# Kernel optimization log

Measured on AMD Instinct MI355X. Metric: run time of the kernel, lower is better.

The kernel has to match this reference:

```python
import jax, jax.numpy as jnp
import numpy as np
from jax import lax

D = 96        # voxel grid side
C = 16        # code_dim == inner channels
NCONV = 17    # total conv layers in the net
DN = ('NCDHW', 'OIDHW', 'NCDHW')
PAD1 = [(1, 1)] * 3


def _bn_relu_mask(y, s, b, mask):
    # eval-mode BN folded to scale/bias, ReLU, then restrict to active voxels
    s = s[None, :, None, None, None]
    b = b[None, :, None, None, None]
    return jnp.maximum(y * s + b, 0.0) * mask


def _subm(x, mask, w, s, b):
    # SubMConv3d: dense 3x3x3 conv on zero-padded sparse features, output only at
    # the (unchanged) active sites -> conv + mask is exactly equal math.
    y = lax.conv_general_dilated(x, w, (1, 1, 1), PAD1, dimension_numbers=DN)
    return _bn_relu_mask(y, s, b, mask)


def _down(x, mask, w, s, b):
    # SparseConv3d stride 2, pad 1: output active wherever any input in the 3^3
    # window is active (= max-pool of the mask).
    y = lax.conv_general_dilated(x, w, (2, 2, 2), PAD1, dimension_numbers=DN)
    new_mask = lax.reduce_window(mask, 0.0, lax.max, (1, 1, 3, 3, 3),
                                 (1, 1, 2, 2, 2),
                                 [(0, 0), (0, 0), (1, 1), (1, 1), (1, 1)])
    return _bn_relu_mask(y, s, b, new_mask), new_mask


def setup_inputs() -> dict:
    key = jax.random.key(0)
    k1, k2, k3, k4, k5 = jax.random.split(key, 5)
    mask_idx = jax.random.randint(k1, (1, 1, D, D, D), 0, 10, dtype=jnp.int32)
    mask = (mask_idx == 0).astype(jnp.float32)
    x = jax.random.normal(k2, (1, C, D, D, D), jnp.float32) * mask
    # 0.05 ~ 1/sqrt(27*16): keeps activations sane over 17 layers
    W = jax.random.normal(k3, (NCONV, C, C, 3, 3, 3), jnp.float32) * 0.05
    bn_scale = jax.random.uniform(k4, (NCONV, C), jnp.float32, 0.5, 1.5)
    bn_bias = jax.random.normal(k5, (NCONV, C), jnp.float32) * 0.1
    return {"x": x, "mask_idx": mask_idx, "W": W,
            "bn_scale": bn_scale, "bn_bias": bn_bias}


def reference(x, mask_idx, W, bn_scale, bn_bias):
    mask = (mask_idx == 0).astype(x.dtype)
    net = x
    i = 0
    # conv0: double_conv at full res
    for _ in range(2):
        net = _subm(net, mask, W[i], bn_scale[i], bn_bias[i]); i += 1
    # down0
    net, mask = _down(net, mask, W[i], bn_scale[i], bn_bias[i]); i += 1
    # conv1: double_conv -> net1.dense()
    for _ in range(2):
        net = _subm(net, mask, W[i], bn_scale[i], bn_bias[i]); i += 1
    net1 = net
    # down1 + conv2 (triple) -> net2
    net, mask = _down(net, mask, W[i], bn_scale[i], bn_bias[i]); i += 1
    for _ in range(3):
        net = _subm(net, mask, W[i], bn_scale[i], bn_bias[i]); i += 1
    net2 = net
    # down2 + conv3 (triple) -> net3
    net, mask = _down(net, mask, W[i], bn_scale[i], bn_bias[i]); i += 1
    for _ in range(3):
        net = _subm(net, mask, W[i], bn_scale[i], bn_bias[i]); i += 1
    net3 = net
    # down3 + conv4 (triple) -> net4
    net, mask = _down(net, mask, W[i], bn_scale[i], bn_bias[i]); i += 1
    for _ in range(3):
        net = _subm(net, mask, W[i], bn_scale[i], bn_bias[i]); i += 1
    net4 = net
    return (net1, net2, net3, net4)
```

## Files before the change

kernel.cpp:

```cpp
#include <hip/hip_runtime.h>

#define C 16
#define TAPS 27
#define NCONV 17
#define LISTCAP 98304
#define NPAIR 14

typedef _Float16 half8 __attribute__((ext_vector_type(8)));
typedef _Float16 half4 __attribute__((ext_vector_type(4)));
typedef float f32x4 __attribute__((ext_vector_type(4)));

__global__ void wh_kernel(const float* __restrict__ W, _Float16* __restrict__ Wh) {
    int i = blockIdx.x * blockDim.x + threadIdx.x;
    const int total = NCONV * NPAIR * 64 * 8;
    if (i >= total) return;
    int j = i & 7;
    int lane = (i >> 3) & 63;
    int p = (i >> 9) % NPAIR;
    int l = (i >> 9) / NPAIR;
    int co = lane & 15;
    int g = lane >> 4;
    int k = 8 * g + j;
    int ci = k & 15;
    int tap = 2 * p + (k >> 4);
    float val = (tap < TAPS) ? W[((l * C + co) * C + ci) * TAPS + tap] : 0.f;
    Wh[i] = (_Float16)val;
}

__global__ void transpose_in_h(const float* __restrict__ x, _Float16* __restrict__ xt, int n) {
    int v = blockIdx.x * blockDim.x + threadIdx.x;
    if (v >= n) return;
    half8 h0, h1;
#pragma unroll
    for (int c = 0; c < 8; c++) h0[c] = (_Float16)x[(long)c * n + v];
#pragma unroll
    for (int c = 0; c < 8; c++) h1[c] = (_Float16)x[(long)(c + 8) * n + v];
    half8* dp = reinterpret_cast<half8*>(xt + (long)v * C);
    dp[0] = h0;
    dp[1] = h1;
}

__global__ void to_ncdhw_h(const _Float16* __restrict__ src, float* __restrict__ dst, int n) {
    int v = blockIdx.x * blockDim.x + threadIdx.x;
    if (v >= n) return;
    const half8* sp = reinterpret_cast<const half8*>(src + (long)v * C);
    half8 q0 = sp[0], q1 = sp[1];
#pragma unroll
    for (int c = 0; c < 8; c++) dst[(long)c * n + v] = (float)q0[c];
#pragma unroll
    for (int c = 0; c < 8; c++) dst[(long)(c + 8) * n + v] = (float)q1[c];
}

__global__ void count_kernel(const int* __restrict__ mi, int* __restrict__ counts, int n) {
    int i = blockIdx.x * 256 + threadIdx.x;
    int act = (i < n) && (mi[i] == 0);
    unsigned long long b = __ballot(act);
    __shared__ int wsum[4];
    int wid = threadIdx.x >> 6, lane = threadIdx.x & 63;
    if (lane == 0) wsum[wid] = __popcll(b);
    __syncthreads();
    if (threadIdx.x == 0) counts[blockIdx.x] = wsum[0] + wsum[1] + wsum[2] + wsum[3];
}

__global__ void scan_kernel(const int* __restrict__ counts, int* __restrict__ offsets,
                            int* __restrict__ nact, int nb) {
    __shared__ int s[256];
    int t = threadIdx.x;
    const int CH = (nb + 255) / 256;
    int base = t * CH, sum = 0;
    for (int j = 0; j < CH; j++)
        if (base + j < nb) sum += counts[base + j];
    s[t] = sum;
    __syncthreads();
    for (int off = 1; off < 256; off <<= 1) {
        int v = (t >= off) ? s[t - off] : 0;
        __syncthreads();
        s[t] += v;
        __syncthreads();
    }
    int run = s[t] - sum;
    for (int j = 0; j < CH; j++) {
        if (base + j < nb) {
            offsets[base + j] = run;
            run += counts[base + j];
        }
    }
    if (t == 255) *nact = s[255];
}

__global__ void scatter_kernel(const int* __restrict__ mi, const int* __restrict__ offsets,
                               int* __restrict__ list, int n, int cap) {
    int i = blockIdx.x * 256 + threadIdx.x;
    int act = (i < n) && (mi[i] == 0);
    unsigned long long b = __ballot(act);
    __shared__ int wsum[4];
    int wid = threadIdx.x >> 6, lane = threadIdx.x & 63;
    if (lane == 0) wsum[wid] = __popcll(b);
    __syncthreads();
    int wbase = 0;
    for (int w = 0; w < wid; w++) wbase += wsum[w];
    int prefix = __popcll(b & ((1ull << lane) - 1));
    if (act) {
        int pos = offsets[blockIdx.x] + wbase + prefix;
        if (pos < cap) list[pos] = i;
    }
}

template <bool FROM_INT>
__global__ void pool_mask_kernel(const int* __restrict__ mi, const float* __restrict__ mf,
                                 float* __restrict__ mout, int Din, int Dout) {
    int i = blockIdx.x * blockDim.x + threadIdx.x;
    int n = Dout * Dout * Dout;
    if (i >= n) return;
    int x = i % Dout, y = (i / Dout) % Dout, z = i / (Dout * Dout);
    float v = 0.f;
    for (int kz = 0; kz < 3; kz++) {
        int zz = 2 * z - 1 + kz;
        if (zz < 0 || zz >= Din) continue;
        for (int ky = 0; ky < 3; ky++) {
            int yy = 2 * y - 1 + ky;
            if (yy < 0 || yy >= Din) continue;
            for (int kx = 0; kx < 3; kx++) {
                int xx = 2 * x - 1 + kx;
                if (xx < 0 || xx >= Din) continue;
                long idx = ((long)zz * Din + yy) * Din + xx;
                float mv = FROM_INT ? ((mi[idx] == 0) ? 1.f : 0.f) : mf[idx];
                v = fmaxf(v, mv);
            }
        }
    }
    mout[i] = v;
}

template <int STRIDE, bool SPARSE>
__global__ __launch_bounds__(256) void mconv_kernel(
    const _Float16* __restrict__ in, _Float16* __restrict__ out,
    const float* __restrict__ mask, const int* __restrict__ list,
    const int* __restrict__ nact, const _Float16* __restrict__ Whl,
    const float* __restrict__ bs, const float* __restrict__ bb,
    int Din, int Dout) {
    int n = Dout * Dout * Dout;
    int nv;
    if (SPARSE) {
        nv = *nact;
        if (nv > LISTCAP) nv = LISTCAP;
    } else {
        nv = n;
    }
    int tile = blockIdx.x * 4 + (threadIdx.x >> 6);
    if (tile * 16 >= nv) return;

    int lane = threadIdx.x & 63;
    int col = lane & 15;
    int g = lane >> 4;
    int s = tile * 16 + col;
    bool val = s < nv;
    int v = 0;
    if (SPARSE) {
        if (val) v = list[s];
    } else {
        v = val ? s : 0;
    }
    int x = v % Dout, y = (v / Dout) % Dout, z = v / (Dout * Dout);

    const half8* wf = reinterpret_cast<const half8*>(Whl);
    half8 a[NPAIR];
#pragma unroll
    for (int p = 0; p < NPAIR; p++) a[p] = wf[p * 64 + lane];

    int half_off = (g & 1) * 8;
    int tg = g >> 1;

    f32x4 acc = {0.f, 0.f, 0.f, 0.f};
#pragma unroll
    for (int p = 0; p < NPAIR; p++) {
        int tap = 2 * p + tg;
        if (tap > TAPS - 1) tap = TAPS - 1;
        int kz = tap / 9, ky = (tap / 3) % 3, kx = tap % 3;
        int zz = STRIDE * z - 1 + kz;
        int yy = STRIDE * y - 1 + ky;
        int xx = STRIDE * x - 1 + kx;
        bool ok = val && ((unsigned)zz < (unsigned)Din) && ((unsigned)yy < (unsigned)Din) &&
                  ((unsigned)xx < (unsigned)Din);
        half8 b = {};
        if (ok) {
            b = *reinterpret_cast<const half8*>(
                in + (long)((zz * Din + yy) * Din + xx) * C + half_off);
        }
        acc = __builtin_amdgcn_mfma_f32_16x16x32_f16(a[p], b, acc, 0, 0, 0);
    }

    if (val) {
        float mk = SPARSE ? 1.f : mask[v];
        int cob = g * 4;
        half4 r;
#pragma unroll
        for (int j = 0; j < 4; j++) {
            float t = fmaxf(acc[j] * bs[cob + j] + bb[cob + j], 0.f) * mk;
            r[j] = (_Float16)t;
        }
        *reinterpret_cast<half4*>(out + (long)v * C + cob) = r;
    }
}

extern "C" void kernel_launch(void* const* d_in, const int* in_sizes, int n_in,
                              void* d_out, int out_size, void* d_ws, size_t ws_size,
                              hipStream_t stream) {
    const float* x = (const float*)d_in[0];
    const int* mask_idx = (const int*)d_in[1];
    const float* W = (const float*)d_in[2];
    const float* bs = (const float*)d_in[3];
    const float* bb = (const float*)d_in[4];
    float* out = (float*)d_out;

    const int n96 = 96 * 96 * 96;
    const int n48 = 48 * 48 * 48;
    const int n24 = 24 * 24 * 24;
    const int n12 = 12 * 12 * 12;
    const int n6 = 6 * 6 * 6;
    const int NB = (n96 + 255) / 256;

    _Float16* P0h = (_Float16*)d_ws;
    _Float16* P1h = P0h + (long)C * n96;
    float* m48 = (float*)(P1h + (long)C * n96);
    float* m24 = m48 + n48;
    float* m12 = m24 + n24;
    float* m6 = m12 + n12;
    _Float16* Wh = (_Float16*)(m6 + n6);
    int* list = (int*)(Wh + (long)NCONV * NPAIR * 64 * 8);
    int* counts = list + LISTCAP;
    int* offsets = counts + NB;
    int* nact = offsets + NB;

    const int BS = 256;
    auto blk = [&](long t) { return dim3((unsigned)((t + BS - 1) / BS)); };
    auto mblk = [&](long nvox) { return dim3((unsigned)((nvox + 63) / 64)); };

    hipMemsetAsync(P1h, 0, (long)C * n96 * sizeof(_Float16), stream);
    hipLaunchKernelGGL(wh_kernel, blk(NCONV * NPAIR * 64 * 8), dim3(BS), 0, stream, W, Wh);
    hipLaunchKernelGGL(transpose_in_h, blk(n96), dim3(BS), 0, stream, x, P0h, n96);
    hipLaunchKernelGGL(count_kernel, dim3(NB), dim3(BS), 0, stream, mask_idx, counts, n96);
    hipLaunchKernelGGL(scan_kernel, dim3(1), dim3(BS), 0, stream, counts, offsets, nact, NB);
    hipLaunchKernelGGL(scatter_kernel, dim3(NB), dim3(BS), 0, stream, mask_idx, offsets, list,
                       n96, LISTCAP);

    auto sconv = [&](const _Float16* in, _Float16* op, int layer) {
        hipLaunchKernelGGL((mconv_kernel<1, true>), mblk(LISTCAP), dim3(BS), 0, stream,
                           in, op, (const float*)nullptr, list, nact,
                           Wh + (long)layer * NPAIR * 64 * 8, bs + layer * C, bb + layer * C,
                           96, 96);
    };
    auto subm = [&](const _Float16* in, _Float16* op, const float* m, int layer, int D) {
        int n = D * D * D;
        hipLaunchKernelGGL((mconv_kernel<1, false>), mblk(n), dim3(BS), 0, stream,
                           in, op, m, list, nact, Wh + (long)layer * NPAIR * 64 * 8,
                           bs + layer * C, bb + layer * C, D, D);
    };
    auto down = [&](const _Float16* in, _Float16* op, const float* m, int layer, int Dout) {
        int n = Dout * Dout * Dout;
        hipLaunchKernelGGL((mconv_kernel<2, false>), mblk(n), dim3(BS), 0, stream,
                           in, op, m, list, nact, Wh + (long)layer * NPAIR * 64 * 8,
                           bs + layer * C, bb + layer * C, 2 * Dout, Dout);
    };

    hipLaunchKernelGGL((pool_mask_kernel<true>), blk(n48), dim3(BS), 0, stream,
                       mask_idx, (const float*)nullptr, m48, 96, 48);
    hipLaunchKernelGGL((pool_mask_kernel<false>), blk(n24), dim3(BS), 0, stream,
                       (const int*)nullptr, m48, m24, 48, 24);
    hipLaunchKernelGGL((pool_mask_kernel<false>), blk(n12), dim3(BS), 0, stream,
                       (const int*)nullptr, m24, m12, 24, 12);
    hipLaunchKernelGGL((pool_mask_kernel<false>), blk(n6), dim3(BS), 0, stream,
                       (const int*)nullptr, m12, m6, 12, 6);

    sconv(P0h, P1h, 0);
    sconv(P1h, P0h, 1);
    down(P0h, P1h, m48, 2, 48);
    subm(P1h, P0h, m48, 3, 48);
    subm(P0h, P1h, m48, 4, 48);
    hipLaunchKernelGGL(to_ncdhw_h, blk(n48), dim3(BS), 0, stream, P1h, out, n48);
    down(P1h, P0h, m24, 5, 24);
    subm(P0h, P1h, m24, 6, 24);
    subm(P1h, P0h, m24, 7, 24);
    subm(P0h, P1h, m24, 8, 24);
    hipLaunchKernelGGL(to_ncdhw_h, blk(n24), dim3(BS), 0, stream, P1h, out + (long)C * n48, n24);
    down(P1h, P0h, m12, 9, 12);
    subm(P0h, P1h, m12, 10, 12);
    subm(P1h, P0h, m12, 11, 12);
    subm(P0h, P1h, m12, 12, 12);
    hipLaunchKernelGGL(to_ncdhw_h, blk(n12), dim3(BS), 0, stream, P1h,
                       out + (long)C * (n48 + n24), n12);
    down(P1h, P0h, m6, 13, 6);
    subm(P0h, P1h, m6, 14, 6);
    subm(P1h, P0h, m6, 15, 6);
    subm(P0h, P1h, m6, 16, 6);
    hipLaunchKernelGGL(to_ncdhw_h, blk(n6), dim3(BS), 0, stream, P1h,
                       out + (long)C * (n48 + n24 + n12), n6);
}
```

Measured before the change: 226.8 us.

## Fuse prep kernels, pooling, NCDHW writes, and low-res tail into single kernels

```diff
diff --git a/kernel.cpp b/kernel.cpp
--- a/kernel.cpp
+++ b/kernel.cpp
@@ -10,56 +10,50 @@
 typedef _Float16 half4 __attribute__((ext_vector_type(4)));
 typedef float f32x4 __attribute__((ext_vector_type(4)));
 
-__global__ void wh_kernel(const float* __restrict__ W, _Float16* __restrict__ Wh) {
-    int i = blockIdx.x * blockDim.x + threadIdx.x;
-    const int total = NCONV * NPAIR * 64 * 8;
-    if (i >= total) return;
-    int j = i & 7;
-    int lane = (i >> 3) & 63;
-    int p = (i >> 9) % NPAIR;
-    int l = (i >> 9) / NPAIR;
-    int co = lane & 15;
-    int g = lane >> 4;
-    int k = 8 * g + j;
-    int ci = k & 15;
-    int tap = 2 * p + (k >> 4);
-    float val = (tap < TAPS) ? W[((l * C + co) * C + ci) * TAPS + tap] : 0.f;
-    Wh[i] = (_Float16)val;
-}
-
-__global__ void transpose_in_h(const float* __restrict__ x, _Float16* __restrict__ xt, int n) {
-    int v = blockIdx.x * blockDim.x + threadIdx.x;
-    if (v >= n) return;
-    half8 h0, h1;
-#pragma unroll
-    for (int c = 0; c < 8; c++) h0[c] = (_Float16)x[(long)c * n + v];
-#pragma unroll
-    for (int c = 0; c < 8; c++) h1[c] = (_Float16)x[(long)(c + 8) * n + v];
-    half8* dp = reinterpret_cast<half8*>(xt + (long)v * C);
-    dp[0] = h0;
-    dp[1] = h1;
-}
-
-__global__ void to_ncdhw_h(const _Float16* __restrict__ src, float* __restrict__ dst, int n) {
-    int v = blockIdx.x * blockDim.x + threadIdx.x;
-    if (v >= n) return;
-    const half8* sp = reinterpret_cast<const half8*>(src + (long)v * C);
-    half8 q0 = sp[0], q1 = sp[1];
-#pragma unroll
-    for (int c = 0; c < 8; c++) dst[(long)c * n + v] = (float)q0[c];
-#pragma unroll
-    for (int c = 0; c < 8; c++) dst[(long)(c + 8) * n + v] = (float)q1[c];
-}
-
-__global__ void count_kernel(const int* __restrict__ mi, int* __restrict__ counts, int n) {
-    int i = blockIdx.x * 256 + threadIdx.x;
-    int act = (i < n) && (mi[i] == 0);
-    unsigned long long b = __ballot(act);
-    __shared__ int wsum[4];
-    int wid = threadIdx.x >> 6, lane = threadIdx.x & 63;
-    if (lane == 0) wsum[wid] = __popcll(b);
-    __syncthreads();
-    if (threadIdx.x == 0) counts[blockIdx.x] = wsum[0] + wsum[1] + wsum[2] + wsum[3];
+__global__ void prep_kernel(const float* __restrict__ x, const int* __restrict__ mask_idx,
+                            _Float16* __restrict__ P0h, _Float16* __restrict__ P1h,
+                            const float* __restrict__ W, _Float16* __restrict__ Wh,
+                            int* __restrict__ counts) {
+    const int n96 = 96 * 96 * 96;
+    int b = blockIdx.x;
+    if (b < 3456) {
+        int v = b * 256 + threadIdx.x;
+        half8 h0, h1;
+#pragma unroll
+        for (int c = 0; c < 8; c++) h0[c] = (_Float16)x[(long)c * n96 + v];
+#pragma unroll
+        for (int c = 0; c < 8; c++) h1[c] = (_Float16)x[(long)(c + 8) * n96 + v];
+        half8* dp = reinterpret_cast<half8*>(P0h + (long)v * C);
+        dp[0] = h0;
+        dp[1] = h1;
+        half8 zz = {};
+        half8* zp = reinterpret_cast<half8*>(P1h + (long)v * C);
+        zp[0] = zz;
+        zp[1] = zz;
+        int act = (mask_idx[v] == 0);
+        unsigned long long bl = __ballot(act);
+        __shared__ int wsum[4];
+        int wid = threadIdx.x >> 6, lane = threadIdx.x & 63;
+        if (lane == 0) wsum[wid] = __popcll(bl);
+        __syncthreads();
+        if (threadIdx.x == 0) counts[b] = wsum[0] + wsum[1] + wsum[2] + wsum[3];
+    } else {
+        int i = (b - 3456) * 256 + threadIdx.x;
+        const int total = NCONV * NPAIR * 64 * 8;
+        if (i < total) {
+            int j = i & 7;
+            int lane = (i >> 3) & 63;
+            int p = (i >> 9) % NPAIR;
+            int l = (i >> 9) / NPAIR;
+            int co = lane & 15;
+            int g = lane >> 4;
+            int k = 8 * g + j;
+            int ci = k & 15;
+            int tap = 2 * p + (k >> 4);
+            float val = (tap < TAPS) ? W[((l * C + co) * C + ci) * TAPS + tap] : 0.f;
+            Wh[i] = (_Float16)val;
+        }
+    }
 }
 
 __global__ void scan_kernel(const int* __restrict__ counts, int* __restrict__ offsets,
@@ -106,39 +100,65 @@
     }
 }
 
-template <bool FROM_INT>
-__global__ void pool_mask_kernel(const int* __restrict__ mi, const float* __restrict__ mf,
-                                 float* __restrict__ mout, int Din, int Dout) {
-    int i = blockIdx.x * blockDim.x + threadIdx.x;
-    int n = Dout * Dout * Dout;
-    if (i >= n) return;
-    int x = i % Dout, y = (i / Dout) % Dout, z = i / (Dout * Dout);
-    float v = 0.f;
-    for (int kz = 0; kz < 3; kz++) {
-        int zz = 2 * z - 1 + kz;
-        if (zz < 0 || zz >= Din) continue;
-        for (int ky = 0; ky < 3; ky++) {
-            int yy = 2 * y - 1 + ky;
-            if (yy < 0 || yy >= Din) continue;
-            for (int kx = 0; kx < 3; kx++) {
-                int xx = 2 * x - 1 + kx;
-                if (xx < 0 || xx >= Din) continue;
-                long idx = ((long)zz * Din + yy) * Din + xx;
-                float mv = FROM_INT ? ((mi[idx] == 0) ? 1.f : 0.f) : mf[idx];
-                v = fmaxf(v, mv);
-            }
-        }
-    }
-    mout[i] = v;
-}
-
-template <int STRIDE, bool SPARSE>
+__global__ void allpools_kernel(const int* __restrict__ mi, float* __restrict__ m48,
+                                float* __restrict__ m24, float* __restrict__ m12,
+                                float* __restrict__ m6) {
+    int b = blockIdx.x;
+    int tid = threadIdx.x;
+    auto rd = [&](int zz, int yy, int xx) -> float {
+        if ((unsigned)zz >= 96u || (unsigned)yy >= 96u || (unsigned)xx >= 96u) return 0.f;
+        return (mi[((long)zz * 96 + yy) * 96 + xx] == 0) ? 1.f : 0.f;
+    };
+    if (b < 432) {
+        int i = b * 256 + tid;
+        int x = i % 48, y = (i / 48) % 48, z = i / (48 * 48);
+        float m = 0.f;
+        for (int dz = 0; dz < 3; dz++)
+            for (int dy = 0; dy < 3; dy++)
+                for (int dx = 0; dx < 3; dx++)
+                    m = fmaxf(m, rd(2 * z - 1 + dz, 2 * y - 1 + dy, 2 * x - 1 + dx));
+        m48[i] = m;
+    } else if (b < 486) {
+        int i = (b - 432) * 256 + tid;
+        int x = i % 24, y = (i / 24) % 24, z = i / (24 * 24);
+        float m = 0.f;
+        for (int dz = 0; dz < 7; dz++)
+            for (int dy = 0; dy < 7; dy++)
+                for (int dx = 0; dx < 7; dx++)
+                    m = fmaxf(m, rd(4 * z - 3 + dz, 4 * y - 3 + dy, 4 * x - 3 + dx));
+        m24[i] = m;
+    } else if (b < 918) {
+        int wv = (b - 486) * 4 + (tid >> 6);
+        int lane = tid & 63;
+        int x = wv % 12, y = (wv / 12) % 12, z = wv / (12 * 12);
+        float m = 0.f;
+        for (int k = lane; k < 3375; k += 64) {
+            int dz = k / 225, r = k % 225, dy = r / 15, dx = r % 15;
+            m = fmaxf(m, rd(8 * z - 7 + dz, 8 * y - 7 + dy, 8 * x - 7 + dx));
+        }
+        for (int off = 32; off; off >>= 1) m = fmaxf(m, __shfl_xor(m, off));
+        if (lane == 0) m12[wv] = m;
+    } else {
+        int wv = (b - 918) * 4 + (tid >> 6);
+        int lane = tid & 63;
+        int x = wv % 6, y = (wv / 6) % 6, z = wv / 36;
+        float m = 0.f;
+        for (int k = lane; k < 29791; k += 64) {
+            int dz = k / 961, r = k % 961, dy = r / 31, dx = r % 31;
+            m = fmaxf(m, rd(16 * z - 15 + dz, 16 * y - 15 + dy, 16 * x - 15 + dx));
+        }
+        for (int off = 32; off; off >>= 1) m = fmaxf(m, __shfl_xor(m, off));
+        if (lane == 0) m6[wv] = m;
+    }
+}
+
+template <int STRIDE, bool SPARSE, bool WF32>
 __global__ __launch_bounds__(256) void mconv_kernel(
     const _Float16* __restrict__ in, _Float16* __restrict__ out,
     const float* __restrict__ mask, const int* __restrict__ list,
     const int* __restrict__ nact, const _Float16* __restrict__ Whl,
     const float* __restrict__ bs, const float* __restrict__ bb,
-    int Din, int Dout) {
+    int Din, int Dout, float* __restrict__ outf) {
     int n = Dout * Dout * Dout;
     int nv;
     if (SPARSE) {
@@ -198,9 +218,88 @@
         for (int j = 0; j < 4; j++) {
             float t = fmaxf(acc[j] * bs[cob + j] + bb[cob + j], 0.f) * mk;
             r[j] = (_Float16)t;
+            if (WF32) outf[(long)(cob + j) * n + v] = t;
         }
         *reinterpret_cast<half4*>(out + (long)v * C + cob) = r;
     }
+}
+
+__global__ __launch_bounds__(512) void fused_tail(
+    const _Float16* __restrict__ gin, const float* __restrict__ m12,
+    const float* __restrict__ m6, const _Float16* __restrict__ Wh,
+    const float* __restrict__ bs, const float* __restrict__ bb,
+    float* __restrict__ out3, float* __restrict__ out4) {
+    extern __shared__ _Float16 lds[];
+    _Float16* H0 = lds;
+    _Float16* H1 = lds + 27648;
+    _Float16* G0 = lds + 55296;
+    _Float16* G1 = lds + 58752;
+
+    int tid = threadIdx.x;
+    int lane = tid & 63;
+    int wid = tid >> 6;
+    int col = lane & 15, g = lane >> 4;
+    int ho = (g & 1) * 8, tg = g >> 1;
+
+    auto layer = [&](const _Float16* ginp, const _Float16* lin, _Float16* lout,
+                     int Din, int Dout, int stride, int lidx,
+                     const float* mk, float* outf) {
+        int n = Dout * Dout * Dout;
+        const half8* wf = reinterpret_cast<const half8*>(Wh + (long)lidx * NPAIR * 64 * 8);
+        half8 a[NPAIR];
+#pragma unroll
+        for (int p = 0; p < NPAIR; p++) a[p] = wf[p * 64 + lane];
+        const float* bsl = bs + lidx * C;
+        const float* bbl = bb + lidx * C;
+        int ntiles = (n + 15) / 16;
+        for (int t = wid; t < ntiles; t += 8) {
+            int s = t * 16 + col;
+            bool val = s < n;
+            int v = val ? s : 0;
+            int x = v % Dout, y = (v / Dout) % Dout, z = v / (Dout * Dout);
+            f32x4 acc = {0.f, 0.f, 0.f, 0.f};
+#pragma unroll
+            for (int p = 0; p < NPAIR; p++) {
+                int tap = 2 * p + tg;
+                if (tap > TAPS - 1) tap = TAPS - 1;
+                int kz = tap / 9, ky = (tap / 3) % 3, kx = tap % 3;
+                int zz = stride * z - 1 + kz;
+                int yy = stride * y - 1 + ky;
+                int xx = stride * x - 1 + kx;
+                bool ok = val && ((unsigned)zz < (unsigned)Din) &&
+                          ((unsigned)yy < (unsigned)Din) && ((unsigned)xx < (unsigned)Din);
+                half8 b = {};
+                if (ok) {
+                    long off = (long)((zz * Din + yy) * Din + xx) * C + ho;
+                    b = ginp ? *reinterpret_cast<const half8*>(ginp + off)
+                             : *reinterpret_cast<const half8*>(lin + off);
+                }
+                acc = __builtin_amdgcn_mfma_f32_16x16x32_f16(a[p], b, acc, 0, 0, 0);
+            }
+            if (val) {
+                float mkv = mk[v];
+                int cob = g * 4;
+                half4 r;
+#pragma unroll
+                for (int j = 0; j < 4; j++) {
+                    float tt = fmaxf(acc[j] * bsl[cob + j] + bbl[cob + j], 0.f) * mkv;
+                    r[j] = (_Float16)tt;
+                    if (outf) outf[(long)(cob + j) * n + v] = tt;
+                }
+                *reinterpret_cast<half4*>(lout + (long)v * C + cob) = r;
+            }
+        }
+        __syncthreads();
+    };
+
+    layer(gin, nullptr, H0, 24, 12, 2, 9, m12, nullptr);
+    layer(nullptr, H0, H1, 12, 12, 1, 10, m12, nullptr);
+    layer(nullptr, H1, H0, 12, 12, 1, 11, m12, nullptr);
+    layer(nullptr, H0, H1, 12, 12, 1, 12, m12, out3);
+    layer(nullptr, H1, G0, 12, 6, 2, 13, m6, nullptr);
+    layer(nullptr, G0, G1, 6, 6, 1, 14, m6, nullptr);
+    layer(nullptr, G1, G0, 6, 6, 1, 15, m6, nullptr);
+    layer(nullptr, G0, G1, 6, 6, 1, 16, m6, out4);
 }
 
 extern "C" void kernel_launch(void* const* d_in, const int* in_sizes, int n_in,
@@ -218,7 +317,7 @@
     const int n24 = 24 * 24 * 24;
     const int n12 = 12 * 12 * 12;
     const int n6 = 6 * 6 * 6;
-    const int NB = (n96 + 255) / 256;
+    const int NB = 3456;
 
     _Float16* P0h = (_Float16*)d_ws;
     _Float16* P1h = P0h + (long)C * n96;
@@ -232,67 +331,49 @@
     int* offsets = counts + NB;
     int* nact = offsets + NB;
 
-    const int BS = 256;
-    auto blk = [&](long t) { return dim3((unsigned)((t + BS - 1) / BS)); };
+    const int LDSB = (2 * 1728 * 16 + 2 * 216 * 16) * (int)sizeof(_Float16);
+    hipFuncSetAttribute(reinterpret_cast<const void*>(&fused_tail),
+                        hipFuncAttributeMaxDynamicSharedMemorySize, LDSB);
+
+    hipLaunchKernelGGL(prep_kernel, dim3(3456 + 476), dim3(256), 0, stream,
+                       x, mask_idx, P0h, P1h, W, Wh, counts);
+    hipLaunchKernelGGL(scan_kernel, dim3(1), dim3(256), 0, stream, counts, offsets, nact, NB);
+    hipLaunchKernelGGL(scatter_kernel, dim3(NB), dim3(256), 0, stream, mask_idx, offsets, list,
+                       n96, LISTCAP);
+    hipLaunchKernelGGL(allpools_kernel, dim3(972), dim3(256), 0, stream,
+                       mask_idx, m48, m24, m12, m6);
+
     auto mblk = [&](long nvox) { return dim3((unsigned)((nvox + 63) / 64)); };
-
-    hipMemsetAsync(P1h, 0, (long)C * n96 * sizeof(_Float16), stream);
-    hipLaunchKernelGGL(wh_kernel, blk(NCONV * NPAIR * 64 * 8), dim3(BS), 0, stream, W, Wh);
-    hipLaunchKernelGGL(transpose_in_h, blk(n96), dim3(BS), 0, stream, x, P0h, n96);
-    hipLaunchKernelGGL(count_kernel, dim3(NB), dim3(BS), 0, stream, mask_idx, counts, n96);
-    hipLaunchKernelGGL(scan_kernel, dim3(1), dim3(BS), 0, stream, counts, offsets, nact, NB);
-    hipLaunchKernelGGL(scatter_kernel, dim3(NB), dim3(BS), 0, stream, mask_idx, offsets, list,
-                       n96, LISTCAP);
-
-    auto sconv = [&](const _Float16* in, _Float16* op, int layer) {
-        hipLaunchKernelGGL((mconv_kernel<1, true>), mblk(LISTCAP), dim3(BS), 0, stream,
-                           in, op, (const float*)nullptr, list, nact,
-                           Wh + (long)layer * NPAIR * 64 * 8, bs + layer * C, bb + layer * C,
-                           96, 96);
-    };
-    auto subm = [&](const _Float16* in, _Float16* op, const float* m, int layer, int D) {
-        int n = D * D * D;
-        hipLaunchKernelGGL((mconv_kernel<1, false>), mblk(n), dim3(BS), 0, stream,
-                           in, op, m, list, nact, Wh + (long)layer * NPAIR * 64 * 8,
-                           bs + layer * C, bb + layer * C, D, D);
-    };
-    auto down = [&](const _Float16* in, _Float16* op, const float* m, int layer, int Dout) {
-        int n = Dout * Dout * Dout;
-        hipLaunchKernelGGL((mconv_kernel<2, false>), mblk(n), dim3(BS), 0, stream,
-                           in, op, m, list, nact, Wh + (long)layer * NPAIR * 64 * 8,
-                           bs + layer * C, bb + layer * C, 2 * Dout, Dout);
-    };
-
-    hipLaunchKernelGGL((pool_mask_kernel<true>), blk(n48), dim3(BS), 0, stream,
-                       mask_idx, (const float*)nullptr, m48, 96, 48);
-    hipLaunchKernelGGL((pool_mask_kernel<false>), blk(n24), dim3(BS), 0, stream,
-                       (const int*)nullptr, m48, m24, 48, 24);
-    hipLaunchKernelGGL((pool_mask_kernel<false>), blk(n12), dim3(BS), 0, stream,
-                       (const int*)nullptr, m24, m12, 24, 12);
-    hipLaunchKernelGGL((pool_mask_kernel<false>), blk(n6), dim3(BS), 0, stream,
-                       (const int*)nullptr, m12, m6, 12, 6);
-
-    sconv(P0h, P1h, 0);
-    sconv(P1h, P0h, 1);
-    down(P0h, P1h, m48, 2, 48);
-    subm(P1h, P0h, m48, 3, 48);
-    subm(P0h, P1h, m48, 4, 48);
-    hipLaunchKernelGGL(to_ncdhw_h, blk(n48), dim3(BS), 0, stream, P1h, out, n48);
-    down(P1h, P0h, m24, 5, 24);
-    subm(P0h, P1h, m24, 6, 24);
-    subm(P1h, P0h, m24, 7, 24);
-    subm(P0h, P1h, m24, 8, 24);
-    hipLaunchKernelGGL(to_ncdhw_h, blk(n24), dim3(BS), 0, stream, P1h, out + (long)C * n48, n24);
-    down(P1h, P0h, m12, 9, 12);
-    subm(P0h, P1h, m12, 10, 12);
-    subm(P1h, P0h, m12, 11, 12);
-    subm(P0h, P1h, m12, 12, 12);
-    hipLaunchKernelGGL(to_ncdhw_h, blk(n12), dim3(BS), 0, stream, P1h,
-                       out + (long)C * (n48 + n24), n12);
-    down(P1h, P0h, m6, 13, 6);
-    subm(P0h, P1h, m6, 14, 6);
-    subm(P1h, P0h, m6, 15, 6);
-    subm(P0h, P1h, m6, 16, 6);
-    hipLaunchKernelGGL(to_ncdhw_h, blk(n6), dim3(BS), 0, stream, P1h,
-                       out + (long)C * (n48 + n24 + n12), n6);
-}
+    auto WL = [&](int l) { return Wh + (long)l * NPAIR * 64 * 8; };
+
+    hipLaunchKernelGGL((mconv_kernel<1, true, false>), mblk(LISTCAP), dim3(256), 0, stream,
+                       P0h, P1h, (const float*)nullptr, list, nact, WL(0), bs, bb, 96, 96,
+                       (float*)nullptr);
+    hipLaunchKernelGGL((mconv_kernel<1, true, false>), mblk(LISTCAP), dim3(256), 0, stream,
+                       P1h, P0h, (const float*)nullptr, list, nact, WL(1), bs + C, bb + C, 96, 96,
+                       (float*)nullptr);
+    hipLaunchKernelGGL((mconv_kernel<2, false, false>), mblk(n48), dim3(256), 0, stream,
+                       P0h, P1h, m48, list, nact, WL(2), bs + 2 * C, bb + 2 * C, 96, 48,
+                       (float*)nullptr);
+    hipLaunchKernelGGL((mconv_kernel<1, false, false>), mblk(n48), dim3(256), 0, stream,
+                       P1h, P0h, m48, list, nact, WL(3), bs + 3 * C, bb + 3 * C, 48, 48,
+                       (float*)nullptr);
+    hipLaunchKernelGGL((mconv_kernel<1, false, true>), mblk(n48), dim3(256), 0, stream,
+                       P0h, P1h, m48, list, nact, WL(4), bs + 4 * C, bb + 4 * C, 48, 48,
+                       out);
+    hipLaunchKernelGGL((mconv_kernel<2, false, false>), mblk(n24), dim3(256), 0, stream,
+                       P1h, P0h, m24, list, nact, WL(5), bs + 5 * C, bb + 5 * C, 48, 24,
+                       (float*)nullptr);
+    hipLaunchKernelGGL((mconv_kernel<1, false, false>), mblk(n24), dim3(256), 0, stream,
+                       P0h, P1h, m24, list, nact, WL(6), bs + 6 * C, bb + 6 * C, 24, 24,
+                       (float*)nullptr);
+    hipLaunchKernelGGL((mconv_kernel<1, false, false>), mblk(n24), dim3(256), 0, stream,
+                       P1h, P0h, m24, list, nact, WL(7), bs + 7 * C, bb + 7 * C, 24, 24,
+                       (float*)nullptr);
+    hipLaunchKernelGGL((mconv_kernel<1, false, true>), mblk(n24), dim3(256), 0, stream,
+                       P0h, P1h, m24, list, nact, WL(8), bs + 8 * C, bb + 8 * C, 24, 24,
+                       out + (long)C * n48);
+    hipLaunchKernelGGL(fused_tail, dim3(1), dim3(512), LDSB, stream,
+                       P1h, m12, m6, Wh, bs, bb,
+                       out + (long)C * (n48 + n24), out + (long)C * (n48 + n24 + n12));
+}
```

Result: slower. 401.9 us (+77.2%).
